# Performance work log

Hardware: AMD Instinct MI355X
Metric: run time of the kernel (lower is better)

The kernel has to match this reference:

```python
import jax, jax.numpy as jnp
import numpy as np

# dims mirroring the torch module: dim=32 (MVN), omega=8, d_head=n_embd//n_head
B, T, E, DH = 8, 2048, 1024, 32
OMEGA, DIM = 8, 32
M = OMEGA * DIM  # 256 random features (omega concatenated N(0, I_dim) samples)


def setup_inputs() -> dict:
    key = jax.random.key(0)
    ks = jax.random.split(key, 8)
    s = 1.0 / np.sqrt(E).astype(np.float32)  # torch Linear-like init scale
    return {
        "x": jax.random.normal(ks[0], (B, T, E), jnp.float32),
        "Wq": jax.random.normal(ks[1], (E, DH), jnp.float32) * s,
        "bq": jax.random.normal(ks[2], (DH,), jnp.float32) * s,
        "Wk": jax.random.normal(ks[3], (E, DH), jnp.float32) * s,
        "bk": jax.random.normal(ks[4], (DH,), jnp.float32) * s,
        "Wv": jax.random.normal(ks[5], (E, DH), jnp.float32) * s,
        "bv": jax.random.normal(ks[6], (DH,), jnp.float32) * s,
        # random-feature matrix: omega stacked samples from N(0, I_DIM) -> [M, DH]
        "w": jax.random.normal(ks[7], (M, DH), jnp.float32),
    }


def reference(x, Wq, bq, Wk, bk, Wv, bv, w):
    # projections (as in Head.forward)
    q = x @ Wq + bq  # [B,T,DH]
    k = x @ Wk + bk  # [B,T,DH]
    v = x @ Wv + bv  # computed but unused, exactly as in the source
    del v
    # Aprox_softmax (FAVOR+-style hyperbolic random features), vectorized per token
    z = k + q                                          # [B,T,DH]
    zsqr = jnp.sum(k * k, -1) + jnp.sum(q * q, -1)     # [B,T]  (per-token norms)
    A = jnp.exp(-0.5 * zsqr)                           # [B,T]
    cosH = jnp.cosh(jnp.einsum('btd,md->btm', z, w))   # [B,T,M]
    R = A[..., None] * cosH                            # [B,T,M]
    return R
```

## Files before the change

### kernel.cpp

```cpp
#include <hip/hip_runtime.h>
#include <cstdint>

#define E_DIM   1024
#define DH      32
#define M_FEAT  256
#define BT      16384

typedef __attribute__((ext_vector_type(8))) short bf16x8;
typedef __attribute__((ext_vector_type(4))) float f32x4;

#define WP_H_OFF 0
#define WP_L_OFF 65536

__device__ __forceinline__ unsigned perm_hi2(unsigned lo_src, unsigned hi_src) {
#if __has_builtin(__builtin_amdgcn_perm)
    return __builtin_amdgcn_perm(hi_src, lo_src, 0x07060302u);
#else
    return (lo_src >> 16) | (hi_src & 0xFFFF0000u);
#endif
}

__device__ __forceinline__ void split2(float f0, float f1, unsigned& ph, unsigned& pl) {
    unsigned u0 = __builtin_bit_cast(unsigned, f0);
    unsigned u1 = __builtin_bit_cast(unsigned, f1);
    ph = perm_hi2(u0, u1);
    float d0 = f0 - __builtin_bit_cast(float, u0 & 0xFFFF0000u);
    float d1 = f1 - __builtin_bit_cast(float, u1 & 0xFFFF0000u);
    pl = perm_hi2(__builtin_bit_cast(unsigned, d0), __builtin_bit_cast(unsigned, d1));
}

__device__ __forceinline__ void split8(const float4& a, const float4& b,
                                       uint4& uh, uint4& ul) {
    split2(a.x, a.y, uh.x, ul.x);
    split2(a.z, a.w, uh.y, ul.y);
    split2(b.x, b.y, uh.z, ul.z);
    split2(b.z, b.w, uh.w, ul.w);
}

__global__ __launch_bounds__(256) void k_prep(
    const float* __restrict__ Wq, const float* __restrict__ Wk,
    short* __restrict__ ws)
{
    __shared__ float wlds[64 * 36];
    const int b = blockIdx.x, tid = threadIdx.x;
    const float* __restrict__ src = (b < 16) ? Wq : Wk;
    const int k0 = (b & 15) * 64;
    const int nbase = (b < 16) ? 0 : 32;
#pragma unroll
    for (int it = 0; it < 2; ++it) {
        int f = it * 256 + tid;
        int k = f >> 3, c4 = f & 7;
        float4 v = *(const float4*)(src + (size_t)(k0 + k) * DH + c4 * 4);
        *(float4*)&wlds[k * 36 + c4 * 4] = v;
    }
    __syncthreads();
    const int n = tid >> 3, kq = tid & 7;
    const int n_g = nbase + n;
    const int nt = n_g >> 4, ln = n_g & 15;
#pragma unroll
    for (int rep = 0; rep < 2; ++rep) {
        int kk = rep * 8 + kq;
        int k_g = k0 + kk * 4;
        float f0 = wlds[(kk * 4 + 0) * 36 + n];
        float f1 = wlds[(kk * 4 + 1) * 36 + n];
        float f2 = wlds[(kk * 4 + 2) * 36 + n];
        float f3 = wlds[(kk * 4 + 3) * 36 + n];
        uint2 ph, pl;
        split2(f0, f1, ph.x, pl.x);
        split2(f2, f3, ph.y, pl.y);
        int sub = k_g >> 5;
        int g = (k_g >> 3) & 3, j0 = k_g & 7;
        int lane = g * 16 + ln;
        size_t flat = ((size_t)(nt * 32 + sub)) * 512 + lane * 8 + j0;
        *(uint2*)(ws + WP_H_OFF + flat) = ph;
        *(uint2*)(ws + WP_L_OFF + flat) = pl;
    }
}

#define TB 32
#define XS2 136
#define QS 68
#define ZS 40

__global__ __launch_bounds__(256, 3) void k_main(
    const float* __restrict__ x, const float* __restrict__ bq,
    const float* __restrict__ bk, const short* __restrict__ ws,
    const float* __restrict__ w, float* __restrict__ out)
{
    __shared__ __align__(16) short xh_s[2][TB * XS2];
    __shared__ __align__(16) short xl_s[2][TB * XS2];
    __shared__ __align__(16) float qk_f[TB * QS];
    __shared__ __align__(16) short zh_s[TB * ZS];
    __shared__ __align__(16) short zl_s[TB * ZS];
    __shared__ float lnA_f[TB];

    const int tid  = threadIdx.x;
    const int lane = tid & 63;
    const int wv   = __builtin_amdgcn_readfirstlane(tid >> 6);
    const int ln15 = lane & 15;
    const int g    = lane >> 4;
    const long t0  = (long)blockIdx.x * TB;

    const int nrow = wv * 16 + ln15;
    const float bias = (nrow < 32) ? bq[nrow] : bk[nrow - 32];

    const int kq = tid & 15;
    const int mr = tid >> 4;

    f32x4 acc0 = {0.f, 0.f, 0.f, 0.f};
    f32x4 acc1 = {0.f, 0.f, 0.f, 0.f};

    const short* wpB_h = ws + WP_H_OFF + (size_t)(wv * 32) * 512 + lane * 8;
    const short* wpB_l = ws + WP_L_OFF + (size_t)(wv * 32) * 512 + lane * 8;
    const float* xr0 = x + (t0 + mr) * (size_t)E_DIM + kq * 8;
    const float* xr1 = x + (t0 + mr + 16) * (size_t)E_DIM + kq * 8;

    float4 a0 = *(const float4*)(xr0 + 0), b0 = *(const float4*)(xr0 + 4);
    float4 a1 = *(const float4*)(xr1 + 0), b1 = *(const float4*)(xr1 + 4);
    {
        uint4 uh, ul;
        split8(a0, b0, uh, ul);
        *(uint4*)&xh_s[0][mr * XS2 + kq * 8] = uh;
        *(uint4*)&xl_s[0][mr * XS2 + kq * 8] = ul;
        split8(a1, b1, uh, ul);
        *(uint4*)&xh_s[0][(mr + 16) * XS2 + kq * 8] = uh;
        *(uint4*)&xl_s[0][(mr + 16) * XS2 + kq * 8] = ul;
    }

#pragma unroll
    for (int p = 0; p < 8; ++p) {
        __syncthreads();
        if (p < 7) {
            a0 = *(const float4*)(xr0 + (p + 1) * 128);
            b0 = *(const float4*)(xr0 + (p + 1) * 128 + 4);
            a1 = *(const float4*)(xr1 + (p + 1) * 128);
            b1 = *(const float4*)(xr1 + (p + 1) * 128 + 4);
        }
#pragma unroll
        for (int j = 0; j < 4; ++j) {
            bf16x8 bh = *(const bf16x8*)(wpB_h + (size_t)(p * 4 + j) * 512);
            bf16x8 bl = *(const bf16x8*)(wpB_l + (size_t)(p * 4 + j) * 512);
            bf16x8 ah0 = *(const bf16x8*)&xh_s[p & 1][ln15 * XS2 + j * 32 + g * 8];
            bf16x8 al0 = *(const bf16x8*)&xl_s[p & 1][ln15 * XS2 + j * 32 + g * 8];
            bf16x8 ah1 = *(const bf16x8*)&xh_s[p & 1][(ln15 + 16) * XS2 + j * 32 + g * 8];
            bf16x8 al1 = *(const bf16x8*)&xl_s[p & 1][(ln15 + 16) * XS2 + j * 32 + g * 8];
            acc0 = __builtin_amdgcn_mfma_f32_16x16x32_bf16(ah0, bh, acc0, 0, 0, 0);
            acc0 = __builtin_amdgcn_mfma_f32_16x16x32_bf16(ah0, bl, acc0, 0, 0, 0);
            acc0 = __builtin_amdgcn_mfma_f32_16x16x32_bf16(al0, bh, acc0, 0, 0, 0);
            acc1 = __builtin_amdgcn_mfma_f32_16x16x32_bf16(ah1, bh, acc1, 0, 0, 0);
            acc1 = __builtin_amdgcn_mfma_f32_16x16x32_bf16(ah1, bl, acc1, 0, 0, 0);
            acc1 = __builtin_amdgcn_mfma_f32_16x16x32_bf16(al1, bh, acc1, 0, 0, 0);
        }
        if (p < 7) {
            uint4 uh, ul;
            split8(a0, b0, uh, ul);
            *(uint4*)&xh_s[(p + 1) & 1][mr * XS2 + kq * 8] = uh;
            *(uint4*)&xl_s[(p + 1) & 1][mr * XS2 + kq * 8] = ul;
            split8(a1, b1, uh, ul);
            *(uint4*)&xh_s[(p + 1) & 1][(mr + 16) * XS2 + kq * 8] = uh;
            *(uint4*)&xl_s[(p + 1) & 1][(mr + 16) * XS2 + kq * 8] = ul;
        }
    }

    float4 wfa[4], wfb[4];
#pragma unroll
    for (int i = 0; i < 4; ++i) {
        const int nf = (wv * 4 + i) * 16 + ln15;
        wfa[i] = *(const float4*)(w + (size_t)nf * DH + g * 8);
        wfb[i] = *(const float4*)(w + (size_t)nf * DH + g * 8 + 4);
    }

#pragma unroll
    for (int r = 0; r < 4; ++r) {
        qk_f[(g * 4 + r) * QS + nrow]        = acc0[r] + bias;
        qk_f[(16 + g * 4 + r) * QS + nrow]   = acc1[r] + bias;
    }
    __syncthreads();

    {
        const int tok = tid >> 3, grp = tid & 7;
        float4 qv = *(const float4*)&qk_f[tok * QS + grp * 4];
        float4 kv = *(const float4*)&qk_f[tok * QS + 32 + grp * 4];
        float z0 = qv.x + kv.x, z1 = qv.y + kv.y, z2 = qv.z + kv.z, z3 = qv.w + kv.w;
        float p = qv.x*qv.x + qv.y*qv.y + qv.z*qv.z + qv.w*qv.w
                + kv.x*kv.x + kv.y*kv.y + kv.z*kv.z + kv.w*kv.w;
        uint2 ph, pl;
        split2(z0, z1, ph.x, pl.x);
        split2(z2, z3, ph.y, pl.y);
        *(uint2*)&zh_s[tok * ZS + grp * 4] = ph;
        *(uint2*)&zl_s[tok * ZS + grp * 4] = pl;
        p += __shfl_xor(p, 1);
        p += __shfl_xor(p, 2);
        p += __shfl_xor(p, 4);
        if (grp == 0) lnA_f[tok] = -0.5f * p;
    }
    __syncthreads();

    f32x4 facc[4][2];
#pragma unroll
    for (int i = 0; i < 4; ++i)
#pragma unroll
        for (int mt = 0; mt < 2; ++mt) facc[i][mt] = (f32x4){0.f,0.f,0.f,0.f};

    bf16x8 a_h[2], a_l[2];
#pragma unroll
    for (int mt = 0; mt < 2; ++mt) {
        a_h[mt] = *(const bf16x8*)&zh_s[(mt * 16 + ln15) * ZS + g * 8];
        a_l[mt] = *(const bf16x8*)&zl_s[(mt * 16 + ln15) * ZS + g * 8];
    }
#pragma unroll
    for (int i = 0; i < 4; ++i) {
        uint4 uh, ul;
        split8(wfa[i], wfb[i], uh, ul);
        bf16x8 wh = __builtin_bit_cast(bf16x8, uh);
        bf16x8 wl = __builtin_bit_cast(bf16x8, ul);
#pragma unroll
        for (int mt = 0; mt < 2; ++mt) {
            facc[i][mt] = __builtin_amdgcn_mfma_f32_16x16x32_bf16(a_h[mt], wh, facc[i][mt], 0, 0, 0);
            facc[i][mt] = __builtin_amdgcn_mfma_f32_16x16x32_bf16(a_h[mt], wl, facc[i][mt], 0, 0, 0);
            facc[i][mt] = __builtin_amdgcn_mfma_f32_16x16x32_bf16(a_l[mt], wh, facc[i][mt], 0, 0, 0);
        }
    }

    float lnAv[2][4];
#pragma unroll
    for (int mt = 0; mt < 2; ++mt)
#pragma unroll
        for (int r = 0; r < 4; ++r) lnAv[mt][r] = lnA_f[mt * 16 + g * 4 + r];

#pragma unroll
    for (int i = 0; i < 4; ++i) {
        const int n = (wv * 4 + i) * 16 + ln15;
#pragma unroll
        for (int mt = 0; mt < 2; ++mt) {
#pragma unroll
            for (int r = 0; r < 4; ++r) {
                float s = facc[i][mt][r];
                float R = 0.5f * (__expf(lnAv[mt][r] + s) + __expf(lnAv[mt][r] - s));
                out[(t0 + mt * 16 + g * 4 + r) * M_FEAT + n] = R;
            }
        }
    }
}

extern "C" void kernel_launch(void* const* d_in, const int* in_sizes, int n_in,
                              void* d_out, int out_size, void* d_ws, size_t ws_size,
                              hipStream_t stream) {
    const float* x  = (const float*)d_in[0];
    const float* Wq = (const float*)d_in[1];
    const float* bq = (const float*)d_in[2];
    const float* Wk = (const float*)d_in[3];
    const float* bk = (const float*)d_in[4];
    const float* w  = (const float*)d_in[7];
    float* out = (float*)d_out;
    short* ws  = (short*)d_ws;

    k_prep<<<dim3(32), dim3(256), 0, stream>>>(Wq, Wk, ws);
    k_main<<<dim3(BT / TB), dim3(256), 0, stream>>>(x, bq, bk, ws, w, out);
}
```

Measured before the change: 121.5 us.

## Load x directly into MFMA A-fragments from global, dropping LDS staging

The projection GEMM no longer stages x through double-buffered LDS with a barrier every K-step. Each wave now loads its own 16-token A fragment straight from global memory into registers, splits it into bf16 hi/lo in registers, and computes two N-tiles, so the waves are split across token halves and column pairs. This removes the LDS traffic and the per-step __syncthreads. In exchange it uses more registers (launch bounds lowered from 3 to 2 blocks) and gives less coalesced global reads of x. Output stores also become nontemporal.

```diff
diff --git a/kernel.cpp b/kernel.cpp
--- a/kernel.cpp
+++ b/kernel.cpp
@@ -69,8 +69,8 @@
         split2(f0, f1, ph.x, pl.x);
         split2(f2, f3, ph.y, pl.y);
         int sub = k_g >> 5;
-        int g = (k_g >> 3) & 3, j0 = k_g & 7;
-        int lane = g * 16 + ln;
+        int gq = (k_g >> 3) & 3, j0 = k_g & 7;
+        int lane = gq * 16 + ln;
         size_t flat = ((size_t)(nt * 32 + sub)) * 512 + lane * 8 + j0;
         *(uint2*)(ws + WP_H_OFF + flat) = ph;
         *(uint2*)(ws + WP_L_OFF + flat) = pl;
@@ -78,17 +78,14 @@
 }
 
 #define TB 32
-#define XS2 136
 #define QS 68
 #define ZS 40
 
-__global__ __launch_bounds__(256, 3) void k_main(
+__global__ __launch_bounds__(256, 2) void k_main(
     const float* __restrict__ x, const float* __restrict__ bq,
     const float* __restrict__ bk, const short* __restrict__ ws,
     const float* __restrict__ w, float* __restrict__ out)
 {
-    __shared__ __align__(16) short xh_s[2][TB * XS2];
-    __shared__ __align__(16) short xl_s[2][TB * XS2];
     __shared__ __align__(16) float qk_f[TB * QS];
     __shared__ __align__(16) short zh_s[TB * ZS];
     __shared__ __align__(16) short zl_s[TB * ZS];
@@ -101,64 +98,57 @@
     const int g    = lane >> 4;
     const long t0  = (long)blockIdx.x * TB;
 
-    const int nrow = wv * 16 + ln15;
-    const float bias = (nrow < 32) ? bq[nrow] : bk[nrow - 32];
-
-    const int kq = tid & 15;
-    const int mr = tid >> 4;
+    const int th = wv >> 1;
+    const int nh = wv & 1;
+
+    const float* __restrict__ xA = x + (t0 + th * 16 + ln15) * (size_t)E_DIM + g * 8;
+    const short* __restrict__ wB0h = ws + WP_H_OFF + (size_t)((nh * 2 + 0) * 32) * 512 + lane * 8;
+    const short* __restrict__ wB0l = ws + WP_L_OFF + (size_t)((nh * 2 + 0) * 32) * 512 + lane * 8;
+    const short* __restrict__ wB1h = ws + WP_H_OFF + (size_t)((nh * 2 + 1) * 32) * 512 + lane * 8;
+    const short* __restrict__ wB1l = ws + WP_L_OFF + (size_t)((nh * 2 + 1) * 32) * 512 + lane * 8;
 
     f32x4 acc0 = {0.f, 0.f, 0.f, 0.f};
     f32x4 acc1 = {0.f, 0.f, 0.f, 0.f};
 
-    const short* wpB_h = ws + WP_H_OFF + (size_t)(wv * 32) * 512 + lane * 8;
-    const short* wpB_l = ws + WP_L_OFF + (size_t)(wv * 32) * 512 + lane * 8;
-    const float* xr0 = x + (t0 + mr) * (size_t)E_DIM + kq * 8;
-    const float* xr1 = x + (t0 + mr + 16) * (size_t)E_DIM + kq * 8;
-
-    float4 a0 = *(const float4*)(xr0 + 0), b0 = *(const float4*)(xr0 + 4);
-    float4 a1 = *(const float4*)(xr1 + 0), b1 = *(const float4*)(xr1 + 4);
-    {
-        uint4 uh, ul;
-        split8(a0, b0, uh, ul);
-        *(uint4*)&xh_s[0][mr * XS2 + kq * 8] = uh;
-        *(uint4*)&xl_s[0][mr * XS2 + kq * 8] = ul;
-        split8(a1, b1, uh, ul);
-        *(uint4*)&xh_s[0][(mr + 16) * XS2 + kq * 8] = uh;
-        *(uint4*)&xl_s[0][(mr + 16) * XS2 + kq * 8] = ul;
-    }
-
+    float4 aCur[4][2], aNxt[4][2];
+#pragma unroll
+    for (int j = 0; j < 4; ++j) {
+        aCur[j][0] = *(const float4*)(xA + j * 32);
+        aCur[j][1] = *(const float4*)(xA + j * 32 + 4);
+    }
 #pragma unroll
     for (int p = 0; p < 8; ++p) {
-        __syncthreads();
         if (p < 7) {
-            a0 = *(const float4*)(xr0 + (p + 1) * 128);
-            b0 = *(const float4*)(xr0 + (p + 1) * 128 + 4);
-            a1 = *(const float4*)(xr1 + (p + 1) * 128);
-            b1 = *(const float4*)(xr1 + (p + 1) * 128 + 4);
+#pragma unroll
+            for (int j = 0; j < 4; ++j) {
+                aNxt[j][0] = *(const float4*)(xA + (p + 1) * 128 + j * 32);
+                aNxt[j][1] = *(const float4*)(xA + (p + 1) * 128 + j * 32 + 4);
+            }
         }
 #pragma unroll
         for (int j = 0; j < 4; ++j) {
-            bf16x8 bh = *(const bf16x8*)(wpB_h + (size_t)(p * 4 + j) * 512);
-            bf16x8 bl = *(const bf16x8*)(wpB_l + (size_t)(p * 4 + j) * 512);
-            bf16x8 ah0 = *(const bf16x8*)&xh_s[p & 1][ln15 * XS2 + j * 32 + g * 8];
-            bf16x8 al0 = *(const bf16x8*)&xl_s[p & 1][ln15 * XS2 + j * 32 + g * 8];
-            bf16x8 ah1 = *(const bf16x8*)&xh_s[p & 1][(ln15 + 16) * XS2 + j * 32 + g * 8];
-            bf16x8 al1 = *(const bf16x8*)&xl_s[p & 1][(ln15 + 16) * XS2 + j * 32 + g * 8];
-            acc0 = __builtin_amdgcn_mfma_f32_16x16x32_bf16(ah0, bh, acc0, 0, 0, 0);
-            acc0 = __builtin_amdgcn_mfma_f32_16x16x32_bf16(ah0, bl, acc0, 0, 0, 0);
-            acc0 = __builtin_amdgcn_mfma_f32_16x16x32_bf16(al0, bh, acc0, 0, 0, 0);
-            acc1 = __builtin_amdgcn_mfma_f32_16x16x32_bf16(ah1, bh, acc1, 0, 0, 0);
-            acc1 = __builtin_amdgcn_mfma_f32_16x16x32_bf16(ah1, bl, acc1, 0, 0, 0);
-            acc1 = __builtin_amdgcn_mfma_f32_16x16x32_bf16(al1, bh, acc1, 0, 0, 0);
+            const size_t off = (size_t)(p * 4 + j) * 512;
+            bf16x8 b0h = *(const bf16x8*)(wB0h + off);
+            bf16x8 b0l = *(const bf16x8*)(wB0l + off);
+            bf16x8 b1h = *(const bf16x8*)(wB1h + off);
+            bf16x8 b1l = *(const bf16x8*)(wB1l + off);
+            uint4 uh, ul;
+            split8(aCur[j][0], aCur[j][1], uh, ul);
+            bf16x8 ah = __builtin_bit_cast(bf16x8, uh);
+            bf16x8 al = __builtin_bit_cast(bf16x8, ul);
+            acc0 = __builtin_amdgcn_mfma_f32_16x16x32_bf16(ah, b0h, acc0, 0, 0, 0);
+            acc0 = __builtin_amdgcn_mfma_f32_16x16x32_bf16(ah, b0l, acc0, 0, 0, 0);
+            acc0 = __builtin_amdgcn_mfma_f32_16x16x32_bf16(al, b0h, acc0, 0, 0, 0);
+            acc1 = __builtin_amdgcn_mfma_f32_16x16x32_bf16(ah, b1h, acc1, 0, 0, 0);
+            acc1 = __builtin_amdgcn_mfma_f32_16x16x32_bf16(ah, b1l, acc1, 0, 0, 0);
+            acc1 = __builtin_amdgcn_mfma_f32_16x16x32_bf16(al, b1h, acc1, 0, 0, 0);
         }
         if (p < 7) {
-            uint4 uh, ul;
-            split8(a0, b0, uh, ul);
-            *(uint4*)&xh_s[(p + 1) & 1][mr * XS2 + kq * 8] = uh;
-            *(uint4*)&xl_s[(p + 1) & 1][mr * XS2 + kq * 8] = ul;
-            split8(a1, b1, uh, ul);
-            *(uint4*)&xh_s[(p + 1) & 1][(mr + 16) * XS2 + kq * 8] = uh;
-            *(uint4*)&xl_s[(p + 1) & 1][(mr + 16) * XS2 + kq * 8] = ul;
+#pragma unroll
+            for (int j = 0; j < 4; ++j) {
+                aCur[j][0] = aNxt[j][0];
+                aCur[j][1] = aNxt[j][1];
+            }
         }
     }
 
@@ -170,10 +160,14 @@
         wfb[i] = *(const float4*)(w + (size_t)nf * DH + g * 8 + 4);
     }
 
+    const int c0 = (nh * 2 + 0) * 16 + ln15;
+    const int c1 = (nh * 2 + 1) * 16 + ln15;
+    const float bias0 = (c0 < 32) ? bq[c0] : bk[c0 - 32];
+    const float bias1 = (c1 < 32) ? bq[c1] : bk[c1 - 32];
 #pragma unroll
     for (int r = 0; r < 4; ++r) {
-        qk_f[(g * 4 + r) * QS + nrow]        = acc0[r] + bias;
-        qk_f[(16 + g * 4 + r) * QS + nrow]   = acc1[r] + bias;
+        qk_f[(th * 16 + g * 4 + r) * QS + c0] = acc0[r] + bias0;
+        qk_f[(th * 16 + g * 4 + r) * QS + c1] = acc1[r] + bias1;
     }
     __syncthreads();
 
@@ -182,17 +176,17 @@
         float4 qv = *(const float4*)&qk_f[tok * QS + grp * 4];
         float4 kv = *(const float4*)&qk_f[tok * QS + 32 + grp * 4];
         float z0 = qv.x + kv.x, z1 = qv.y + kv.y, z2 = qv.z + kv.z, z3 = qv.w + kv.w;
-        float p = qv.x*qv.x + qv.y*qv.y + qv.z*qv.z + qv.w*qv.w
-                + kv.x*kv.x + kv.y*kv.y + kv.z*kv.z + kv.w*kv.w;
+        float pw = qv.x*qv.x + qv.y*qv.y + qv.z*qv.z + qv.w*qv.w
+                 + kv.x*kv.x + kv.y*kv.y + kv.z*kv.z + kv.w*kv.w;
         uint2 ph, pl;
         split2(z0, z1, ph.x, pl.x);
         split2(z2, z3, ph.y, pl.y);
         *(uint2*)&zh_s[tok * ZS + grp * 4] = ph;
         *(uint2*)&zl_s[tok * ZS + grp * 4] = pl;
-        p += __shfl_xor(p, 1);
-        p += __shfl_xor(p, 2);
-        p += __shfl_xor(p, 4);
-        if (grp == 0) lnA_f[tok] = -0.5f * p;
+        pw += __shfl_xor(pw, 1);
+        pw += __shfl_xor(pw, 2);
+        pw += __shfl_xor(pw, 4);
+        if (grp == 0) lnA_f[tok] = -0.5f * pw;
     }
     __syncthreads();
 
@@ -237,7 +231,7 @@
             for (int r = 0; r < 4; ++r) {
                 float s = facc[i][mt][r];
                 float R = 0.5f * (__expf(lnAv[mt][r] + s) + __expf(lnAv[mt][r] - s));
-                out[(t0 + mt * 16 + g * 4 + r) * M_FEAT + n] = R;
+                __builtin_nontemporal_store(R, &out[(t0 + mt * 16 + g * 4 + r) * M_FEAT + n]);
             }
         }
     }
```

Result: slower. 139.5 us (+14.8%).

## Halve token tile to 16 per block, raise occupancy, use nontemporal output stores

Applied to the files above, without the earlier changes.

Shrinks each block from 32 to 16 tokens, which removes the second accumulator set and row loads. This doubles the grid and lets launch bounds target 4 waves per SIMD. The intent is more blocks in flight to hide the memory latency of streaming x and writing the output. Output stores now use nontemporal hints to avoid polluting cache. In exchange, each block amortizes the packed Wq/Wk fragment loads and the w loads over fewer tokens, so weight traffic per token doubles, and half the threads sit idle in the z-computation step.

```diff
diff --git a/kernel.cpp b/kernel.cpp
--- a/kernel.cpp
+++ b/kernel.cpp
@@ -69,20 +69,20 @@
         split2(f0, f1, ph.x, pl.x);
         split2(f2, f3, ph.y, pl.y);
         int sub = k_g >> 5;
-        int g = (k_g >> 3) & 3, j0 = k_g & 7;
-        int lane = g * 16 + ln;
+        int gq = (k_g >> 3) & 3, j0 = k_g & 7;
+        int lane = gq * 16 + ln;
         size_t flat = ((size_t)(nt * 32 + sub)) * 512 + lane * 8 + j0;
         *(uint2*)(ws + WP_H_OFF + flat) = ph;
         *(uint2*)(ws + WP_L_OFF + flat) = pl;
     }
 }
 
-#define TB 32
+#define TB 16
 #define XS2 136
 #define QS 68
 #define ZS 40
 
-__global__ __launch_bounds__(256, 3) void k_main(
+__global__ __launch_bounds__(256, 4) void k_main(
     const float* __restrict__ x, const float* __restrict__ bq,
     const float* __restrict__ bk, const short* __restrict__ ws,
     const float* __restrict__ w, float* __restrict__ out)
@@ -108,23 +108,17 @@
     const int mr = tid >> 4;
 
     f32x4 acc0 = {0.f, 0.f, 0.f, 0.f};
-    f32x4 acc1 = {0.f, 0.f, 0.f, 0.f};
 
     const short* wpB_h = ws + WP_H_OFF + (size_t)(wv * 32) * 512 + lane * 8;
     const short* wpB_l = ws + WP_L_OFF + (size_t)(wv * 32) * 512 + lane * 8;
     const float* xr0 = x + (t0 + mr) * (size_t)E_DIM + kq * 8;
-    const float* xr1 = x + (t0 + mr + 16) * (size_t)E_DIM + kq * 8;
 
     float4 a0 = *(const float4*)(xr0 + 0), b0 = *(const float4*)(xr0 + 4);
-    float4 a1 = *(const float4*)(xr1 + 0), b1 = *(const float4*)(xr1 + 4);
     {
         uint4 uh, ul;
         split8(a0, b0, uh, ul);
         *(uint4*)&xh_s[0][mr * XS2 + kq * 8] = uh;
         *(uint4*)&xl_s[0][mr * XS2 + kq * 8] = ul;
-        split8(a1, b1, uh, ul);
-        *(uint4*)&xh_s[0][(mr + 16) * XS2 + kq * 8] = uh;
-        *(uint4*)&xl_s[0][(mr + 16) * XS2 + kq * 8] = ul;
     }
 
 #pragma unroll
@@ -133,8 +127,6 @@
         if (p < 7) {
             a0 = *(const float4*)(xr0 + (p + 1) * 128);
             b0 = *(const float4*)(xr0 + (p + 1) * 128 + 4);
-            a1 = *(const float4*)(xr1 + (p + 1) * 128);
-            b1 = *(const float4*)(xr1 + (p + 1) * 128 + 4);
         }
 #pragma unroll
         for (int j = 0; j < 4; ++j) {
@@ -142,23 +134,15 @@
             bf16x8 bl = *(const bf16x8*)(wpB_l + (size_t)(p * 4 + j) * 512);
             bf16x8 ah0 = *(const bf16x8*)&xh_s[p & 1][ln15 * XS2 + j * 32 + g * 8];
             bf16x8 al0 = *(const bf16x8*)&xl_s[p & 1][ln15 * XS2 + j * 32 + g * 8];
-            bf16x8 ah1 = *(const bf16x8*)&xh_s[p & 1][(ln15 + 16) * XS2 + j * 32 + g * 8];
-            bf16x8 al1 = *(const bf16x8*)&xl_s[p & 1][(ln15 + 16) * XS2 + j * 32 + g * 8];
             acc0 = __builtin_amdgcn_mfma_f32_16x16x32_bf16(ah0, bh, acc0, 0, 0, 0);
             acc0 = __builtin_amdgcn_mfma_f32_16x16x32_bf16(ah0, bl, acc0, 0, 0, 0);
             acc0 = __builtin_amdgcn_mfma_f32_16x16x32_bf16(al0, bh, acc0, 0, 0, 0);
-            acc1 = __builtin_amdgcn_mfma_f32_16x16x32_bf16(ah1, bh, acc1, 0, 0, 0);
-            acc1 = __builtin_amdgcn_mfma_f32_16x16x32_bf16(ah1, bl, acc1, 0, 0, 0);
-            acc1 = __builtin_amdgcn_mfma_f32_16x16x32_bf16(al1, bh, acc1, 0, 0, 0);
         }
         if (p < 7) {
             uint4 uh, ul;
             split8(a0, b0, uh, ul);
             *(uint4*)&xh_s[(p + 1) & 1][mr * XS2 + kq * 8] = uh;
             *(uint4*)&xl_s[(p + 1) & 1][mr * XS2 + kq * 8] = ul;
-            split8(a1, b1, uh, ul);
-            *(uint4*)&xh_s[(p + 1) & 1][(mr + 16) * XS2 + kq * 8] = uh;
-            *(uint4*)&xl_s[(p + 1) & 1][(mr + 16) * XS2 + kq * 8] = ul;
         }
     }
 
@@ -172,73 +156,58 @@
 
 #pragma unroll
     for (int r = 0; r < 4; ++r) {
-        qk_f[(g * 4 + r) * QS + nrow]        = acc0[r] + bias;
-        qk_f[(16 + g * 4 + r) * QS + nrow]   = acc1[r] + bias;
+        qk_f[(g * 4 + r) * QS + nrow] = acc0[r] + bias;
     }
     __syncthreads();
 
-    {
+    if (tid < 128) {
         const int tok = tid >> 3, grp = tid & 7;
         float4 qv = *(const float4*)&qk_f[tok * QS + grp * 4];
         float4 kv = *(const float4*)&qk_f[tok * QS + 32 + grp * 4];
         float z0 = qv.x + kv.x, z1 = qv.y + kv.y, z2 = qv.z + kv.z, z3 = qv.w + kv.w;
-        float p = qv.x*qv.x + qv.y*qv.y + qv.z*qv.z + qv.w*qv.w
-                + kv.x*kv.x + kv.y*kv.y + kv.z*kv.z + kv.w*kv.w;
+        float pw = qv.x*qv.x + qv.y*qv.y + qv.z*qv.z + qv.w*qv.w
+                 + kv.x*kv.x + kv.y*kv.y + kv.z*kv.z + kv.w*kv.w;
         uint2 ph, pl;
         split2(z0, z1, ph.x, pl.x);
         split2(z2, z3, ph.y, pl.y);
         *(uint2*)&zh_s[tok * ZS + grp * 4] = ph;
         *(uint2*)&zl_s[tok * ZS + grp * 4] = pl;
-        p += __shfl_xor(p, 1);
-        p += __shfl_xor(p, 2);
-        p += __shfl_xor(p, 4);
-        if (grp == 0) lnA_f[tok] = -0.5f * p;
+        pw += __shfl_xor(pw, 1);
+        pw += __shfl_xor(pw, 2);
+        pw += __shfl_xor(pw, 4);
+        if (grp == 0) lnA_f[tok] = -0.5f * pw;
     }
     __syncthreads();
 
-    f32x4 facc[4][2];
-#pragma unroll
-    for (int i = 0; i < 4; ++i)
-#pragma unroll
-        for (int mt = 0; mt < 2; ++mt) facc[i][mt] = (f32x4){0.f,0.f,0.f,0.f};
-
-    bf16x8 a_h[2], a_l[2];
-#pragma unroll
-    for (int mt = 0; mt < 2; ++mt) {
-        a_h[mt] = *(const bf16x8*)&zh_s[(mt * 16 + ln15) * ZS + g * 8];
-        a_l[mt] = *(const bf16x8*)&zl_s[(mt * 16 + ln15) * ZS + g * 8];
-    }
+    f32x4 facc[4];
+#pragma unroll
+    for (int i = 0; i < 4; ++i) facc[i] = (f32x4){0.f,0.f,0.f,0.f};
+
+    bf16x8 a_h = *(const bf16x8*)&zh_s[ln15 * ZS + g * 8];
+    bf16x8 a_l = *(const bf16x8*)&zl_s[ln15 * ZS + g * 8];
 #pragma unroll
     for (int i = 0; i < 4; ++i) {
         uint4 uh, ul;
         split8(wfa[i], wfb[i], uh, ul);
         bf16x8 wh = __builtin_bit_cast(bf16x8, uh);
         bf16x8 wl = __builtin_bit_cast(bf16x8, ul);
-#pragma unroll
-        for (int mt = 0; mt < 2; ++mt) {
-            facc[i][mt] = __builtin_amdgcn_mfma_f32_16x16x32_bf16(a_h[mt], wh, facc[i][mt], 0, 0, 0);
-            facc[i][mt] = __builtin_amdgcn_mfma_f32_16x16x32_bf16(a_h[mt], wl, facc[i][mt], 0, 0, 0);
-            facc[i][mt] = __builtin_amdgcn_mfma_f32_16x16x32_bf16(a_l[mt], wh, facc[i][mt], 0, 0, 0);
-        }
-    }
-
-    float lnAv[2][4];
-#pragma unroll
-    for (int mt = 0; mt < 2; ++mt)
-#pragma unroll
-        for (int r = 0; r < 4; ++r) lnAv[mt][r] = lnA_f[mt * 16 + g * 4 + r];
+        facc[i] = __builtin_amdgcn_mfma_f32_16x16x32_bf16(a_h, wh, facc[i], 0, 0, 0);
+        facc[i] = __builtin_amdgcn_mfma_f32_16x16x32_bf16(a_h, wl, facc[i], 0, 0, 0);
+        facc[i] = __builtin_amdgcn_mfma_f32_16x16x32_bf16(a_l, wh, facc[i], 0, 0, 0);
+    }
+
+    float lnAv[4];
+#pragma unroll
+    for (int r = 0; r < 4; ++r) lnAv[r] = lnA_f[g * 4 + r];
 
 #pragma unroll
     for (int i = 0; i < 4; ++i) {
         const int n = (wv * 4 + i) * 16 + ln15;
 #pragma unroll
-        for (int mt = 0; mt < 2; ++mt) {
-#pragma unroll
-            for (int r = 0; r < 4; ++r) {
-                float s = facc[i][mt][r];
-                float R = 0.5f * (__expf(lnAv[mt][r] + s) + __expf(lnAv[mt][r] - s));
-                out[(t0 + mt * 16 + g * 4 + r) * M_FEAT + n] = R;
-            }
+        for (int r = 0; r < 4; ++r) {
+            float s = facc[i][r];
+            float R = 0.5f * (__expf(lnAv[r] + s) + __expf(lnAv[r] - s));
+            __builtin_nontemporal_store(R, &out[(t0 + g * 4 + r) * M_FEAT + n]);
         }
     }
 }
```

New measurement: 125.5 us. +3.3%, slower.

## Switch split-precision MFMA from 3-term bf16 to 2-term fp16 with nontemporal stores

Applied to the files above, without the earlier changes.

Replaces the bf16 hi/lo splitting (three MFMAs per tile: hh, hl, lh) with fp16 splitting of the activations only. The weights become a single fp16 value, so each tile needs two MFMAs and loads half the weight data. This cuts MFMA count and prep-workspace traffic, but the weights are rounded to fp16 precision and large activations could lose range. Output stores are also made nontemporal to reduce cache pollution.

```diff
diff --git a/kernel.cpp b/kernel.cpp
--- a/kernel.cpp
+++ b/kernel.cpp
@@ -6,35 +6,29 @@
 #define M_FEAT  256
 #define BT      16384
 
-typedef __attribute__((ext_vector_type(8))) short bf16x8;
+typedef __attribute__((ext_vector_type(8))) _Float16 f16x8;
 typedef __attribute__((ext_vector_type(4))) float f32x4;
 
-#define WP_H_OFF 0
-#define WP_L_OFF 65536
-
-__device__ __forceinline__ unsigned perm_hi2(unsigned lo_src, unsigned hi_src) {
-#if __has_builtin(__builtin_amdgcn_perm)
-    return __builtin_amdgcn_perm(hi_src, lo_src, 0x07060302u);
-#else
-    return (lo_src >> 16) | (hi_src & 0xFFFF0000u);
-#endif
-}
-
-__device__ __forceinline__ void split2(float f0, float f1, unsigned& ph, unsigned& pl) {
-    unsigned u0 = __builtin_bit_cast(unsigned, f0);
-    unsigned u1 = __builtin_bit_cast(unsigned, f1);
-    ph = perm_hi2(u0, u1);
-    float d0 = f0 - __builtin_bit_cast(float, u0 & 0xFFFF0000u);
-    float d1 = f1 - __builtin_bit_cast(float, u1 & 0xFFFF0000u);
-    pl = perm_hi2(__builtin_bit_cast(unsigned, d0), __builtin_bit_cast(unsigned, d1));
-}
-
-__device__ __forceinline__ void split8(const float4& a, const float4& b,
-                                       uint4& uh, uint4& ul) {
-    split2(a.x, a.y, uh.x, ul.x);
-    split2(a.z, a.w, uh.y, ul.y);
-    split2(b.x, b.y, uh.z, ul.z);
-    split2(b.z, b.w, uh.w, ul.w);
+
+__device__ __forceinline__ unsigned packh2(_Float16 a, _Float16 b) {
+    union { _Float16 h[2]; unsigned u; } t;
+    t.h[0] = a; t.h[1] = b;
+    return t.u;
+}
+
+__device__ __forceinline__ void splitf16_2(float f0, float f1, unsigned& ph, unsigned& pl) {
+    _Float16 h0 = (_Float16)f0, h1 = (_Float16)f1;
+    float l0 = f0 - (float)h0, l1 = f1 - (float)h1;
+    ph = packh2(h0, h1);
+    pl = packh2((_Float16)l0, (_Float16)l1);
+}
+
+__device__ __forceinline__ void splitf16_8(const float4& a, const float4& b,
+                                           uint4& uh, uint4& ul) {
+    splitf16_2(a.x, a.y, uh.x, ul.x);
+    splitf16_2(a.z, a.w, uh.y, ul.y);
+    splitf16_2(b.x, b.y, uh.z, ul.z);
+    splitf16_2(b.z, b.w, uh.w, ul.w);
 }
 
 __global__ __launch_bounds__(256) void k_prep(
@@ -65,15 +59,14 @@
         float f1 = wlds[(kk * 4 + 1) * 36 + n];
         float f2 = wlds[(kk * 4 + 2) * 36 + n];
         float f3 = wlds[(kk * 4 + 3) * 36 + n];
-        uint2 ph, pl;
-        split2(f0, f1, ph.x, pl.x);
-        split2(f2, f3, ph.y, pl.y);
+        uint2 ph;
+        ph.x = packh2((_Float16)f0, (_Float16)f1);
+        ph.y = packh2((_Float16)f2, (_Float16)f3);
         int sub = k_g >> 5;
-        int g = (k_g >> 3) & 3, j0 = k_g & 7;
-        int lane = g * 16 + ln;
+        int gq = (k_g >> 3) & 3, j0 = k_g & 7;
+        int lane = gq * 16 + ln;
         size_t flat = ((size_t)(nt * 32 + sub)) * 512 + lane * 8 + j0;
-        *(uint2*)(ws + WP_H_OFF + flat) = ph;
-        *(uint2*)(ws + WP_L_OFF + flat) = pl;
+        *(uint2*)(ws + flat) = ph;
     }
 }
 
@@ -110,8 +103,7 @@
     f32x4 acc0 = {0.f, 0.f, 0.f, 0.f};
     f32x4 acc1 = {0.f, 0.f, 0.f, 0.f};
 
-    const short* wpB_h = ws + WP_H_OFF + (size_t)(wv * 32) * 512 + lane * 8;
-    const short* wpB_l = ws + WP_L_OFF + (size_t)(wv * 32) * 512 + lane * 8;
+    const short* wpB = ws + (size_t)(wv * 32) * 512 + lane * 8;
     const float* xr0 = x + (t0 + mr) * (size_t)E_DIM + kq * 8;
     const float* xr1 = x + (t0 + mr + 16) * (size_t)E_DIM + kq * 8;
 
@@ -119,10 +111,10 @@
     float4 a1 = *(const float4*)(xr1 + 0), b1 = *(const float4*)(xr1 + 4);
     {
         uint4 uh, ul;
-        split8(a0, b0, uh, ul);
+        splitf16_8(a0, b0, uh, ul);
         *(uint4*)&xh_s[0][mr * XS2 + kq * 8] = uh;
         *(uint4*)&xl_s[0][mr * XS2 + kq * 8] = ul;
-        split8(a1, b1, uh, ul);
+        splitf16_8(a1, b1, uh, ul);
         *(uint4*)&xh_s[0][(mr + 16) * XS2 + kq * 8] = uh;
         *(uint4*)&xl_s[0][(mr + 16) * XS2 + kq * 8] = ul;
     }
@@ -138,25 +130,22 @@
         }
 #pragma unroll
         for (int j = 0; j < 4; ++j) {
-            bf16x8 bh = *(const bf16x8*)(wpB_h + (size_t)(p * 4 + j) * 512);
-            bf16x8 bl = *(const bf16x8*)(wpB_l + (size_t)(p * 4 + j) * 512);
-            bf16x8 ah0 = *(const bf16x8*)&xh_s[p & 1][ln15 * XS2 + j * 32 + g * 8];
-            bf16x8 al0 = *(const bf16x8*)&xl_s[p & 1][ln15 * XS2 + j * 32 + g * 8];
-            bf16x8 ah1 = *(const bf16x8*)&xh_s[p & 1][(ln15 + 16) * XS2 + j * 32 + g * 8];
-            bf16x8 al1 = *(const bf16x8*)&xl_s[p & 1][(ln15 + 16) * XS2 + j * 32 + g * 8];
-            acc0 = __builtin_amdgcn_mfma_f32_16x16x32_bf16(ah0, bh, acc0, 0, 0, 0);
-            acc0 = __builtin_amdgcn_mfma_f32_16x16x32_bf16(ah0, bl, acc0, 0, 0, 0);
-            acc0 = __builtin_amdgcn_mfma_f32_16x16x32_bf16(al0, bh, acc0, 0, 0, 0);
-            acc1 = __builtin_amdgcn_mfma_f32_16x16x32_bf16(ah1, bh, acc1, 0, 0, 0);
-            acc1 = __builtin_amdgcn_mfma_f32_16x16x32_bf16(ah1, bl, acc1, 0, 0, 0);
-            acc1 = __builtin_amdgcn_mfma_f32_16x16x32_bf16(al1, bh, acc1, 0, 0, 0);
+            f16x8 bh = *(const f16x8*)(wpB + (size_t)(p * 4 + j) * 512);
+            f16x8 ah0 = *(const f16x8*)&xh_s[p & 1][ln15 * XS2 + j * 32 + g * 8];
+            f16x8 al0 = *(const f16x8*)&xl_s[p & 1][ln15 * XS2 + j * 32 + g * 8];
+            f16x8 ah1 = *(const f16x8*)&xh_s[p & 1][(ln15 + 16) * XS2 + j * 32 + g * 8];
+            f16x8 al1 = *(const f16x8*)&xl_s[p & 1][(ln15 + 16) * XS2 + j * 32 + g * 8];
+            acc0 = __builtin_amdgcn_mfma_f32_16x16x32_f16(ah0, bh, acc0, 0, 0, 0);
+            acc0 = __builtin_amdgcn_mfma_f32_16x16x32_f16(al0, bh, acc0, 0, 0, 0);
+            acc1 = __builtin_amdgcn_mfma_f32_16x16x32_f16(ah1, bh, acc1, 0, 0, 0);
+            acc1 = __builtin_amdgcn_mfma_f32_16x16x32_f16(al1, bh, acc1, 0, 0, 0);
         }
         if (p < 7) {
             uint4 uh, ul;
-            split8(a0, b0, uh, ul);
+            splitf16_8(a0, b0, uh, ul);
             *(uint4*)&xh_s[(p + 1) & 1][mr * XS2 + kq * 8] = uh;
             *(uint4*)&xl_s[(p + 1) & 1][mr * XS2 + kq * 8] = ul;
-            split8(a1, b1, uh, ul);
+            splitf16_8(a1, b1, uh, ul);
             *(uint4*)&xh_s[(p + 1) & 1][(mr + 16) * XS2 + kq * 8] = uh;
             *(uint4*)&xl_s[(p + 1) & 1][(mr + 16) * XS2 + kq * 8] = ul;
         }
@@ -182,17 +171,17 @@
         float4 qv = *(const float4*)&qk_f[tok * QS + grp * 4];
         float4 kv = *(const float4*)&qk_f[tok * QS + 32 + grp * 4];
         float z0 = qv.x + kv.x, z1 = qv.y + kv.y, z2 = qv.z + kv.z, z3 = qv.w + kv.w;
-        float p = qv.x*qv.x + qv.y*qv.y + qv.z*qv.z + qv.w*qv.w
-                + kv.x*kv.x + kv.y*kv.y + kv.z*kv.z + kv.w*kv.w;
+        float pw = qv.x*qv.x + qv.y*qv.y + qv.z*qv.z + qv.w*qv.w
+                 + kv.x*kv.x + kv.y*kv.y + kv.z*kv.z + kv.w*kv.w;
         uint2 ph, pl;
-        split2(z0, z1, ph.x, pl.x);
-        split2(z2, z3, ph.y, pl.y);
+        splitf16_2(z0, z1, ph.x, pl.x);
+        splitf16_2(z2, z3, ph.y, pl.y);
         *(uint2*)&zh_s[tok * ZS + grp * 4] = ph;
         *(uint2*)&zl_s[tok * ZS + grp * 4] = pl;
-        p += __shfl_xor(p, 1);
-        p += __shfl_xor(p, 2);
-        p += __shfl_xor(p, 4);
-        if (grp == 0) lnA_f[tok] = -0.5f * p;
+        pw += __shfl_xor(pw, 1);
+        pw += __shfl_xor(pw, 2);
+        pw += __shfl_xor(pw, 4);
+        if (grp == 0) lnA_f[tok] = -0.5f * pw;
     }
     __syncthreads();
 
@@ -202,23 +191,24 @@
 #pragma unroll
         for (int mt = 0; mt < 2; ++mt) facc[i][mt] = (f32x4){0.f,0.f,0.f,0.f};
 
-    bf16x8 a_h[2], a_l[2];
+    f16x8 a_h[2], a_l[2];
 #pragma unroll
     for (int mt = 0; mt < 2; ++mt) {
-        a_h[mt] = *(const bf16x8*)&zh_s[(mt * 16 + ln15) * ZS + g * 8];
-        a_l[mt] = *(const bf16x8*)&zl_s[(mt * 16 + ln15) * ZS + g * 8];
+        a_h[mt] = *(const f16x8*)&zh_s[(mt * 16 + ln15) * ZS + g * 8];
+        a_l[mt] = *(const f16x8*)&zl_s[(mt * 16 + ln15) * ZS + g * 8];
     }
 #pragma unroll
     for (int i = 0; i < 4; ++i) {
-        uint4 uh, ul;
-        split8(wfa[i], wfb[i], uh, ul);
-        bf16x8 wh = __builtin_bit_cast(bf16x8, uh);
-        bf16x8 wl = __builtin_bit_cast(bf16x8, ul);
+        uint4 uw;
+        uw.x = packh2((_Float16)wfa[i].x, (_Float16)wfa[i].y);
+        uw.y = packh2((_Float16)wfa[i].z, (_Float16)wfa[i].w);
+        uw.z = packh2((_Float16)wfb[i].x, (_Float16)wfb[i].y);
+        uw.w = packh2((_Float16)wfb[i].z, (_Float16)wfb[i].w);
+        f16x8 w8 = __builtin_bit_cast(f16x8, uw);
 #pragma unroll
         for (int mt = 0; mt < 2; ++mt) {
-            facc[i][mt] = __builtin_amdgcn_mfma_f32_16x16x32_bf16(a_h[mt], wh, facc[i][mt], 0, 0, 0);
-            facc[i][mt] = __builtin_amdgcn_mfma_f32_16x16x32_bf16(a_h[mt], wl, facc[i][mt], 0, 0, 0);
-            facc[i][mt] = __builtin_amdgcn_mfma_f32_16x16x32_bf16(a_l[mt], wh, facc[i][mt], 0, 0, 0);
+            facc[i][mt] = __builtin_amdgcn_mfma_f32_16x16x32_f16(a_h[mt], w8, facc[i][mt], 0, 0, 0);
+            facc[i][mt] = __builtin_amdgcn_mfma_f32_16x16x32_f16(a_l[mt], w8, facc[i][mt], 0, 0, 0);
         }
     }
 
@@ -237,7 +227,7 @@
             for (int r = 0; r < 4; ++r) {
                 float s = facc[i][mt][r];
                 float R = 0.5f * (__expf(lnAv[mt][r] + s) + __expf(lnAv[mt][r] - s));
-                out[(t0 + mt * 16 + g * 4 + r) * M_FEAT + n] = R;
+                __builtin_nontemporal_store(R, &out[(t0 + mt * 16 + g * 4 + r) * M_FEAT + n]);
             }
         }
     }
```

Measured after the change: 120.9 us. Within noise of the previous version (-0.5%).
